# Optimization experiments

Measured on AMD Instinct MI355X. Metric: run time of the kernel, lower is better.

The kernel has to match this reference:

```python
import jax, jax.numpy as jnp
import numpy as np

N_SPATIAL = 65160
N_SPHERE = 2883
N_EDGES = 131072
D = 256             # latent_size
EDGE_IN_FIRST = 3 + 2 * D   # raw 3-dim displacements + sender + receiver = 515
EDGE_IN_REST = 3 * D        # after step 1 edges are D-dim = 768
NODE_IN = 2 * D
N_STEPS = 3


def _layernorm(x, g, b, eps=1e-5):
    m = jnp.mean(x, axis=-1, keepdims=True)
    v = jnp.var(x, axis=-1, keepdims=True)
    return (x - m) * jax.lax.rsqrt(v + eps) * g + b


def _mlp(x, W1, b1, g, o, W2, b2):
    # Linear -> relu -> LayerNorm -> Linear (matches hk.Sequential)
    h = jax.nn.relu(x @ W1 + b1)
    return _layernorm(h, g, o) @ W2 + b2


def setup_inputs() -> dict:
    key = jax.random.key(0)
    ks = jax.random.split(key, 12)

    def glorot(k, shape):
        return jax.random.normal(k, shape, jnp.float32) / np.sqrt(shape[0]).astype(np.float32)

    nodes = jax.random.normal(ks[0], (N_SPATIAL + N_SPHERE, D), jnp.float32)
    edges = jax.random.normal(ks[1], (N_EDGES, 3), jnp.float32)
    senders = jax.random.randint(ks[2], (N_EDGES,), 0, N_SPATIAL)
    # receivers index into the sphere portion of the concatenated node array
    receivers = jax.random.randint(ks[3], (N_EDGES,), 0, N_SPHERE) + N_SPATIAL
    return {
        "nodes": nodes,
        "edges": edges,
        "senders": senders,
        "receivers": receivers,
        "We1a": glorot(ks[4], (EDGE_IN_FIRST, D)),
        "We1b": glorot(ks[5], (EDGE_IN_REST, D)),
        "be1": jnp.zeros((D,), jnp.float32),
        "ge": jnp.ones((D,), jnp.float32),
        "oe": jnp.zeros((D,), jnp.float32),
        "We2": glorot(ks[6], (D, D)),
        "be2": jnp.zeros((D,), jnp.float32),
        "Wn1": glorot(ks[7], (NODE_IN, D)),
        "bn1": jnp.zeros((D,), jnp.float32),
        "gn": jnp.ones((D,), jnp.float32),
        "on": jnp.zeros((D,), jnp.float32),
        "Wn2": glorot(ks[8], (D, D)),
        "bn2": jnp.zeros((D,), jnp.float32),
        "n_spatial": N_SPATIAL,
        "n_sphere": N_SPHERE,
    }


def reference(nodes, edges, senders, receivers,
              We1a, We1b, be1, ge, oe, We2, be2,
              Wn1, bn1, gn, on, Wn2, bn2,
              n_spatial, n_sphere):
    recv_ids = receivers - n_spatial  # local sphere indices in [0, n_sphere)
    for step in range(N_STEPS):
        s = nodes[senders]                                   # [E, D]
        r = nodes[receivers]                                 # [E, D]
        edge_in = jnp.concatenate([edges, s, r], axis=1)     # [E, 3+2D] or [E, 3D]
        W1 = We1a if step == 0 else We1b
        edges = _mlp(edge_in, W1, be1, ge, oe, We2, be2)     # [E, D]
        messages = jax.ops.segment_sum(edges, recv_ids, num_segments=n_sphere)  # [S, D]
        sphere = nodes[n_spatial:]                           # [S, D]
        node_in = jnp.concatenate([sphere, messages], axis=1)
        updated = _mlp(node_in, Wn1, bn1, gn, on, Wn2, bn2)  # [S, D]
        nodes = jnp.concatenate([nodes[:n_spatial], updated], axis=0)
    return nodes[n_spatial:]
```

## Files before the change

kernel.cpp:

```cpp
#include <hip/hip_runtime.h>
#include <hip/hip_bf16.h>
#include <cstdint>
#include <cstddef>

#define N_SPATIAL_C 65160
#define N_SPHERE_C  2883
#define N_EDGES_C   131072

typedef short bf16x8 __attribute__((ext_vector_type(8)));
typedef float f32x4  __attribute__((ext_vector_type(4)));

__device__ inline float bf2f(ushort u) {
    union { uint u; float f; } c; c.u = ((uint)u) << 16; return c.f;
}
__device__ inline ushort f2bf(float f) {
    __hip_bfloat16 h = __float2bfloat16(f);
    union { __hip_bfloat16 h; ushort u; } c; c.h = h; return c.u;
}

template<int EPI, int KI, typename OutT>
__global__ __launch_bounds__(256, 2) void mfma_gemm(
    const ushort* __restrict__ A, const ushort* __restrict__ Bt,
    OutT* __restrict__ C, int M,
    const float* __restrict__ bias,
    const float* __restrict__ g, const float* __restrict__ o,
    const ushort* __restrict__ P, const int* __restrict__ senders,
    const float* __restrict__ Rf, const int* __restrict__ receivers)
{
    constexpr int CHR = KI / 8;
    __shared__ __align__(16) ushort Atile[64 * KI];

    const int m0   = blockIdx.x * 64;
    const int t    = threadIdx.x;
    const int w    = t >> 6;
    const int lane = t & 63;
    const int lo   = lane & 15, hi = lane >> 4, sw = lo & 7;
    const int bn   = w * 64;

#pragma unroll
    for (int i = 0; i < (64 * CHR) / 256; ++i) {
        int ci = i * 256 + t;
        int r  = ci / CHR;
        int cs = ci % CHR;
        int cg = cs ^ (r & 7);
        int rg = m0 + r; if (rg >= M) rg = M - 1;
        const ushort* gp = A + (size_t)rg * KI + cg * 8;
        const ushort* lp = Atile + (size_t)(i * 256 + w * 64) * 8;
        __builtin_amdgcn_global_load_lds(
            (const __attribute__((address_space(1))) unsigned int*)gp,
            (__attribute__((address_space(3))) unsigned int*)lp, 16, 0, 0);
    }
    __syncthreads();

    f32x4 acc[4][4];
#pragma unroll
    for (int rt = 0; rt < 4; ++rt)
#pragma unroll
        for (int ct = 0; ct < 4; ++ct)
#pragma unroll
            for (int j = 0; j < 4; ++j) acc[rt][ct][j] = 0.f;

#pragma unroll
    for (int ks = 0; ks < KI / 32; ++ks) {
        bf16x8 av[4], bv[4];
#pragma unroll
        for (int rt = 0; rt < 4; ++rt) {
            int row = rt * 16 + lo;
            av[rt] = *reinterpret_cast<const bf16x8*>(
                Atile + ((size_t)row * CHR + ((ks * 4 + hi) ^ sw)) * 8);
        }
#pragma unroll
        for (int ct = 0; ct < 4; ++ct)
            bv[ct] = *reinterpret_cast<const bf16x8*>(
                Bt + (size_t)(bn + ct * 16 + lo) * KI + ks * 32 + hi * 8);
#pragma unroll
        for (int rt = 0; rt < 4; ++rt)
#pragma unroll
            for (int ct = 0; ct < 4; ++ct)
                acc[rt][ct] = __builtin_amdgcn_mfma_f32_16x16x32_bf16(
                    av[rt], bv[ct], acc[rt][ct], 0, 0, 0);
    }

    float* xbuf = reinterpret_cast<float*>(Atile);
    const int rl = t >> 4, q = t & 15, c0 = q * 16;

#pragma unroll
    for (int ph = 0; ph < 4; ++ph) {
        __syncthreads();
#pragma unroll
        for (int ct = 0; ct < 4; ++ct)
#pragma unroll
            for (int reg = 0; reg < 4; ++reg)
                xbuf[(size_t)(hi * 4 + reg) * 260 + (bn + ct * 16 + lo)] =
                    acc[ph][ct][reg];
        __syncthreads();

        int rowg = m0 + ph * 16 + rl;
        bool ok  = rowg < M;
        int rowc = ok ? rowg : M - 1;

        float x[16];
#pragma unroll
        for (int jj = 0; jj < 4; ++jj) {
            f32x4 v = *reinterpret_cast<const f32x4*>(xbuf + (size_t)rl * 260 + c0 + jj * 4);
            x[jj*4+0] = v[0]; x[jj*4+1] = v[1]; x[jj*4+2] = v[2]; x[jj*4+3] = v[3];
        }
        if (bias) {
#pragma unroll
            for (int jj = 0; jj < 4; ++jj) {
                f32x4 v = *reinterpret_cast<const f32x4*>(bias + c0 + jj * 4);
                x[jj*4+0] += v[0]; x[jj*4+1] += v[1]; x[jj*4+2] += v[2]; x[jj*4+3] += v[3];
            }
        }
        if (EPI == 2) {
            int sIdx = senders[rowc];
            int rIdx = receivers[rowc] - N_SPATIAL_C;
            bf16x8 p0 = *reinterpret_cast<const bf16x8*>(P + (size_t)sIdx * 256 + c0);
            bf16x8 p1 = *reinterpret_cast<const bf16x8*>(P + (size_t)sIdx * 256 + c0 + 8);
#pragma unroll
            for (int j = 0; j < 8; ++j) {
                x[j]     += bf2f((ushort)p0[j]);
                x[8 + j] += bf2f((ushort)p1[j]);
            }
#pragma unroll
            for (int jj = 0; jj < 4; ++jj) {
                f32x4 v = *reinterpret_cast<const f32x4*>(Rf + (size_t)rIdx * 256 + c0 + jj * 4);
                x[jj*4+0] += v[0]; x[jj*4+1] += v[1]; x[jj*4+2] += v[2]; x[jj*4+3] += v[3];
            }
        }
        if (EPI >= 1) {
#pragma unroll
            for (int j = 0; j < 16; ++j) x[j] = fmaxf(x[j], 0.f);
            float s1 = 0.f, s2 = 0.f;
#pragma unroll
            for (int j = 0; j < 16; ++j) { s1 += x[j]; s2 += x[j] * x[j]; }
#pragma unroll
            for (int m = 1; m < 16; m <<= 1) {
                s1 += __shfl_xor(s1, m);
                s2 += __shfl_xor(s2, m);
            }
            float mean = s1 * (1.f / 256.f);
            float var  = s2 * (1.f / 256.f) - mean * mean;
            float rstd = rsqrtf(var + 1e-5f);
            float gg[16], oo[16];
#pragma unroll
            for (int jj = 0; jj < 4; ++jj) {
                f32x4 gv = *reinterpret_cast<const f32x4*>(g + c0 + jj * 4);
                f32x4 ov = *reinterpret_cast<const f32x4*>(o + c0 + jj * 4);
                gg[jj*4+0]=gv[0]; gg[jj*4+1]=gv[1]; gg[jj*4+2]=gv[2]; gg[jj*4+3]=gv[3];
                oo[jj*4+0]=ov[0]; oo[jj*4+1]=ov[1]; oo[jj*4+2]=ov[2]; oo[jj*4+3]=ov[3];
            }
#pragma unroll
            for (int j = 0; j < 16; ++j)
                x[j] = (x[j] - mean) * rstd * gg[j] + oo[j];
        }
        if (ok) {
            if constexpr (sizeof(OutT) == 2) {
                bf16x8 s0, s1;
#pragma unroll
                for (int j = 0; j < 8; ++j) {
                    s0[j] = (short)f2bf(x[j]);
                    s1[j] = (short)f2bf(x[8 + j]);
                }
                ushort* Cp = (ushort*)C + (size_t)rowg * 256 + c0;
                *reinterpret_cast<bf16x8*>(Cp)     = s0;
                *reinterpret_cast<bf16x8*>(Cp + 8) = s1;
            } else {
                float* Cp = (float*)C + (size_t)rowg * 256 + c0;
#pragma unroll
                for (int jj = 0; jj < 4; ++jj) {
                    f32x4 v;
                    v[0]=x[jj*4+0]; v[1]=x[jj*4+1]; v[2]=x[jj*4+2]; v[3]=x[jj*4+3];
                    *reinterpret_cast<f32x4*>(Cp + jj * 4) = v;
                }
            }
        }
    }
}

__global__ __launch_bounds__(256) void fuse0(
    const float* __restrict__ edges3, const float* __restrict__ Ae,
    const ushort* __restrict__ P, const int* __restrict__ senders,
    const float* __restrict__ Rf, const int* __restrict__ receivers,
    const float* __restrict__ be1, const float* __restrict__ g,
    const float* __restrict__ o, ushort* __restrict__ H)
{
    int row  = blockIdx.x * 4 + (threadIdx.x >> 6);
    int lane = threadIdx.x & 63;
    int c = lane * 4;

    float e0 = edges3[(size_t)row * 3 + 0];
    float e1 = edges3[(size_t)row * 3 + 1];
    float e2 = edges3[(size_t)row * 3 + 2];
    int s = senders[row];
    int r = receivers[row] - N_SPATIAL_C;
    ushort4 pv = *reinterpret_cast<const ushort4*>(P + (size_t)s * 256 + c);
    float4  rv = *reinterpret_cast<const float4*>(Rf + (size_t)r * 256 + c);

    float pw[4] = {bf2f(pv.x), bf2f(pv.y), bf2f(pv.z), bf2f(pv.w)};
    float rw[4] = {rv.x, rv.y, rv.z, rv.w};
    float x[4];
#pragma unroll
    for (int j = 0; j < 4; ++j) {
        x[j] = e0 * Ae[c + j] + e1 * Ae[256 + c + j] + e2 * Ae[512 + c + j]
             + be1[c + j] + pw[j] + rw[j];
        x[j] = fmaxf(x[j], 0.f);
    }
    float s1 = x[0] + x[1] + x[2] + x[3];
    float s2 = x[0]*x[0] + x[1]*x[1] + x[2]*x[2] + x[3]*x[3];
#pragma unroll
    for (int m = 32; m > 0; m >>= 1) { s1 += __shfl_xor(s1, m); s2 += __shfl_xor(s2, m); }
    float mean = s1 * (1.f / 256.f);
    float var  = s2 * (1.f / 256.f) - mean * mean;
    float rstd = rsqrtf(var + 1e-5f);
#pragma unroll
    for (int j = 0; j < 4; ++j) {
        float y = (x[j] - mean) * rstd * g[c + j] + o[c + j];
        H[(size_t)row * 256 + c + j] = f2bf(y);
    }
}

__global__ void count_k(const int* __restrict__ receivers, int* __restrict__ cnt)
{
    int e = blockIdx.x * 256 + threadIdx.x;
    if (e < N_EDGES_C) atomicAdd(&cnt[receivers[e] - N_SPATIAL_C], 1);
}

__global__ void scan_k(const int* __restrict__ cnt, int* __restrict__ row_start)
{
    __shared__ int sums[257];
    const int CH = 12;
    int t = threadIdx.x;
    int local = 0;
    for (int i = 0; i < CH; ++i) {
        int idx = t * CH + i;
        if (idx < N_SPHERE_C) local += cnt[idx];
    }
    sums[t] = local;
    __syncthreads();
    if (t == 0) {
        int run = 0;
        for (int i = 0; i < 256; ++i) { int v = sums[i]; sums[i] = run; run += v; }
        sums[256] = run;
    }
    __syncthreads();
    int base = sums[t];
    for (int i = 0; i < CH; ++i) {
        int idx = t * CH + i;
        if (idx < N_SPHERE_C) { row_start[idx] = base; base += cnt[idx]; }
    }
    if (t == 0) row_start[N_SPHERE_C] = sums[256];
}

__global__ void fill_k(const int* __restrict__ receivers, const int* __restrict__ row_start,
                       int* __restrict__ cursor, int* __restrict__ csr)
{
    int e = blockIdx.x * 256 + threadIdx.x;
    if (e < N_EDGES_C) {
        int rid = receivers[e] - N_SPATIAL_C;
        int pos = atomicAdd(&cursor[rid], 1);
        csr[row_start[rid] + pos] = e;
    }
}

__global__ __launch_bounds__(256) void seg_gather(
    const ushort* __restrict__ H, const int* __restrict__ row_start,
    const int* __restrict__ csr, ushort* __restrict__ S)
{
    __shared__ float red[3][64][4];
    int n = blockIdx.x;
    int sub = threadIdx.x >> 6, l = threadIdx.x & 63, c = l * 4;
    int beg = row_start[n], end = row_start[n + 1];
    float a0 = 0.f, a1 = 0.f, a2 = 0.f, a3 = 0.f;
    for (int i = beg + sub; i < end; i += 4) {
        int e = csr[i];
        ushort4 v = *reinterpret_cast<const ushort4*>(H + (size_t)e * 256 + c);
        a0 += bf2f(v.x); a1 += bf2f(v.y); a2 += bf2f(v.z); a3 += bf2f(v.w);
    }
    if (sub) { red[sub-1][l][0]=a0; red[sub-1][l][1]=a1; red[sub-1][l][2]=a2; red[sub-1][l][3]=a3; }
    __syncthreads();
    if (sub == 0) {
#pragma unroll
        for (int s_ = 0; s_ < 3; ++s_) {
            a0 += red[s_][l][0]; a1 += red[s_][l][1];
            a2 += red[s_][l][2]; a3 += red[s_][l][3];
        }
        ushort4 u; u.x = f2bf(a0); u.y = f2bf(a1); u.z = f2bf(a2); u.w = f2bf(a3);
        *reinterpret_cast<ushort4*>(S + (size_t)n * 256 + c) = u;
    }
}

__global__ void node_assemble(const ushort* __restrict__ sphere, const float* __restrict__ Mmsg,
                              const int* __restrict__ cnt, const float* __restrict__ be2,
                              ushort* __restrict__ node_in)
{
    int n = blockIdx.x, d = threadIdx.x;
    node_in[(size_t)n * 512 + d] = sphere[(size_t)n * 256 + d];
    node_in[(size_t)n * 512 + 256 + d] =
        f2bf(Mmsg[(size_t)n * 256 + d] + (float)cnt[n] * be2[d]);
}

__global__ __launch_bounds__(256) void wf_kernel(
    const float* __restrict__ We2, const float* __restrict__ Be, ushort* __restrict__ Wft)
{
    __shared__ float colB[256];
    int j = blockIdx.x, k = threadIdx.x;
    colB[k] = Be[(size_t)k * 256 + j];
    __syncthreads();
    const float* wrow = We2 + (size_t)k * 256;
    float acc = 0.f;
    for (int t = 0; t < 256; ++t) acc += wrow[t] * colB[t];
    Wft[(size_t)j * 256 + k] = f2bf(acc);
}

__global__ void bf_kernel(const float* __restrict__ be1, const float* __restrict__ be2,
                          const float* __restrict__ Be, float* __restrict__ bfc)
{
    int j = threadIdx.x;
    float acc = be1[j];
    for (int k = 0; k < 256; ++k) acc += be2[k] * Be[(size_t)k * 256 + j];
    bfc[j] = acc;
}

__global__ void tcast(const float* __restrict__ W, ushort* __restrict__ Wt, int K)
{
    __shared__ float tbuf[16][17];
    int k0 = blockIdx.x * 16, n0 = blockIdx.y * 16;
    int tx = threadIdx.x, ty = threadIdx.y;
    tbuf[ty][tx] = W[(size_t)(k0 + ty) * 256 + n0 + tx];
    __syncthreads();
    Wt[(size_t)(n0 + ty) * K + k0 + tx] = f2bf(tbuf[tx][ty]);
}

__global__ void cast_f32_bf16(const float* __restrict__ src, ushort* __restrict__ dst, int n4)
{
    int i = blockIdx.x * 256 + threadIdx.x;
    if (i < n4) {
        float4 v = *reinterpret_cast<const float4*>(src + (size_t)i * 4);
        ushort4 u;
        u.x = f2bf(v.x); u.y = f2bf(v.y); u.z = f2bf(v.z); u.w = f2bf(v.w);
        *reinterpret_cast<ushort4*>(dst + (size_t)i * 4) = u;
    }
}

extern "C" void kernel_launch(void* const* d_in, const int* in_sizes, int n_in,
                              void* d_out, int out_size, void* d_ws, size_t ws_size,
                              hipStream_t stream)
{
    const float* nodes     = (const float*)d_in[0];
    const float* edges3    = (const float*)d_in[1];
    const int*   senders   = (const int*)d_in[2];
    const int*   receivers = (const int*)d_in[3];
    const float* We1a      = (const float*)d_in[4];
    const float* We1b      = (const float*)d_in[5];
    const float* be1       = (const float*)d_in[6];
    const float* ge        = (const float*)d_in[7];
    const float* oe        = (const float*)d_in[8];
    const float* We2       = (const float*)d_in[9];
    const float* be2       = (const float*)d_in[10];
    const float* Wn1       = (const float*)d_in[11];
    const float* bn1       = (const float*)d_in[12];
    const float* gn        = (const float*)d_in[13];
    const float* on_       = (const float*)d_in[14];
    const float* Wn2       = (const float*)d_in[15];
    const float* bn2       = (const float*)d_in[16];

    const float* Ae  = We1a;
    const float* As_ = We1a + 3 * 256;
    const float* Ar  = We1a + 259 * 256;
    const float* Be  = We1b;
    const float* Bs_ = We1b + 256 * 256;
    const float* Br  = We1b + 512 * 256;

    char* ws = (char*)d_ws;
    size_t off = 0;
    auto alloc = [&](size_t b) -> char* {
        char* p = ws + off;
        off += (b + 255) & ~(size_t)255;
        return p;
    };
    ushort* H          = (ushort*)alloc((size_t)N_EDGES_C * 256 * 2);
    ushort* Pb         = (ushort*)alloc((size_t)N_SPATIAL_C * 256 * 2);
    ushort* nodes_bf   = (ushort*)alloc((size_t)N_SPATIAL_C * 256 * 2);
    float*  Rf         = (float*)alloc((size_t)N_SPHERE_C * 256 * 4);
    ushort* sphere_bf  = (ushort*)alloc((size_t)N_SPHERE_C * 256 * 2);
    ushort* S_bf       = (ushort*)alloc((size_t)N_SPHERE_C * 256 * 2);
    ushort* nH         = (ushort*)alloc((size_t)N_SPHERE_C * 256 * 2);
    ushort* node_in_bf = (ushort*)alloc((size_t)N_SPHERE_C * 512 * 2);
    float*  Mmsg       = (float*)alloc((size_t)N_SPHERE_C * 256 * 4);
    ushort* Ast  = (ushort*)alloc(256 * 256 * 2);
    ushort* Art  = (ushort*)alloc(256 * 256 * 2);
    ushort* Bst  = (ushort*)alloc(256 * 256 * 2);
    ushort* Brt  = (ushort*)alloc(256 * 256 * 2);
    ushort* We2t = (ushort*)alloc(256 * 256 * 2);
    ushort* Wn2t = (ushort*)alloc(256 * 256 * 2);
    ushort* Wn1t = (ushort*)alloc(512 * 256 * 2);
    ushort* Wft  = (ushort*)alloc(256 * 256 * 2);
    float*  bfc  = (float*)alloc(256 * 4);
    int* cnt       = (int*)alloc(N_SPHERE_C * 4);
    int* cursor    = (int*)alloc(N_SPHERE_C * 4);
    int* row_start = (int*)alloc((N_SPHERE_C + 1) * 4);
    int* csr       = (int*)alloc((size_t)N_EDGES_C * 4);

    hipMemsetAsync(cnt, 0, N_SPHERE_C * 4, stream);
    hipMemsetAsync(cursor, 0, N_SPHERE_C * 4, stream);
    count_k<<<(N_EDGES_C + 255) / 256, 256, 0, stream>>>(receivers, cnt);
    scan_k<<<1, 256, 0, stream>>>(cnt, row_start);
    fill_k<<<(N_EDGES_C + 255) / 256, 256, 0, stream>>>(receivers, row_start, cursor, csr);

    dim3 tb(16, 16);
    tcast<<<dim3(16, 16), tb, 0, stream>>>(As_, Ast, 256);
    tcast<<<dim3(16, 16), tb, 0, stream>>>(Ar,  Art, 256);
    tcast<<<dim3(16, 16), tb, 0, stream>>>(Bs_, Bst, 256);
    tcast<<<dim3(16, 16), tb, 0, stream>>>(Br,  Brt, 256);
    tcast<<<dim3(16, 16), tb, 0, stream>>>(We2, We2t, 256);
    tcast<<<dim3(16, 16), tb, 0, stream>>>(Wn2, Wn2t, 256);
    tcast<<<dim3(32, 16), tb, 0, stream>>>(Wn1, Wn1t, 512);
    wf_kernel<<<256, 256, 0, stream>>>(We2, Be, Wft);
    bf_kernel<<<1, 256, 0, stream>>>(be1, be2, Be, bfc);

    cast_f32_bf16<<<(N_SPATIAL_C * 64 + 255) / 256, 256, 0, stream>>>(
        nodes, nodes_bf, N_SPATIAL_C * 64);
    cast_f32_bf16<<<(N_SPHERE_C * 64 + 255) / 256, 256, 0, stream>>>(
        nodes + (size_t)N_SPATIAL_C * 256, sphere_bf, N_SPHERE_C * 64);

    const int GE = N_EDGES_C / 64;
    const int GP = (N_SPATIAL_C + 63) / 64;
    const int GS = (N_SPHERE_C + 63) / 64;

    mfma_gemm<0, 256, ushort><<<GP, 256, 0, stream>>>(
        nodes_bf, Ast, Pb, N_SPATIAL_C,
        nullptr, nullptr, nullptr, nullptr, nullptr, nullptr, nullptr);

    for (int step = 0; step < 3; ++step) {
        mfma_gemm<0, 256, float><<<GS, 256, 0, stream>>>(
            sphere_bf, step == 0 ? Art : Brt, Rf, N_SPHERE_C,
            nullptr, nullptr, nullptr, nullptr, nullptr, nullptr, nullptr);

        if (step == 0) {
            fuse0<<<N_EDGES_C / 4, 256, 0, stream>>>(
                edges3, Ae, Pb, senders, Rf, receivers, be1, ge, oe, H);
            mfma_gemm<0, 256, ushort><<<GP, 256, 0, stream>>>(
                nodes_bf, Bst, Pb, N_SPATIAL_C,
                nullptr, nullptr, nullptr, nullptr, nullptr, nullptr, nullptr);
        } else {
            mfma_gemm<2, 256, ushort><<<GE, 256, 0, stream>>>(
                H, Wft, H, N_EDGES_C,
                bfc, ge, oe, Pb, senders, Rf, receivers);
        }

        seg_gather<<<N_SPHERE_C, 256, 0, stream>>>(H, row_start, csr, S_bf);
        mfma_gemm<0, 256, float><<<GS, 256, 0, stream>>>(
            S_bf, We2t, Mmsg, N_SPHERE_C,
            nullptr, nullptr, nullptr, nullptr, nullptr, nullptr, nullptr);
        node_assemble<<<N_SPHERE_C, 256, 0, stream>>>(sphere_bf, Mmsg, cnt, be2, node_in_bf);

        mfma_gemm<1, 512, ushort><<<GS, 256, 0, stream>>>(
            node_in_bf, Wn1t, nH, N_SPHERE_C,
            bn1, gn, on_, nullptr, nullptr, nullptr, nullptr);
        if (step < 2) {
            mfma_gemm<0, 256, ushort><<<GS, 256, 0, stream>>>(
                nH, Wn2t, sphere_bf, N_SPHERE_C,
                bn2, nullptr, nullptr, nullptr, nullptr, nullptr, nullptr);
        } else {
            mfma_gemm<0, 256, float><<<GS, 256, 0, stream>>>(
                nH, Wn2t, (float*)d_out, N_SPHERE_C,
                bn2, nullptr, nullptr, nullptr, nullptr, nullptr, nullptr);
        }
    }
}
```

Measured before the change: 677.6 us.

## Make big GEMMs persistent with double-buffered A tiles and fold message GEMM into node MLP

The large GEMMs (spatial projections and the edge MLP) now run as persistent kernels over a fixed 512-block grid. Each block keeps its B fragments in registers and double-buffers A tiles in LDS, with explicit waitcnt and barriers so the next tile's load overlaps the current tile's compute. Separately, the We2 message projection is folded algebraically into the node-MLP first-layer weights, with a count-weighted bias vector added in the epilogue. seg_gather and the weight GEMMs now write straight into a strided node_in buffer, which removes the Mmsg GEMM, node_assemble, and extra copies. The costs are higher register and LDS pressure and possible bf16 rounding changes from the precomputed weight product.

```diff
diff --git a/kernel.cpp b/kernel.cpp
--- a/kernel.cpp
+++ b/kernel.cpp
@@ -18,163 +18,217 @@
     union { __hip_bfloat16 h; ushort u; } c; c.h = h; return c.u;
 }
 
-template<int EPI, int KI, typename OutT>
+#define VMWAIT8()  asm volatile("s_waitcnt vmcnt(8)" ::: "memory")
+#define VMWAIT0()  asm volatile("s_waitcnt vmcnt(0)" ::: "memory")
+#define LGKM0()    asm volatile("s_waitcnt lgkmcnt(0)" ::: "memory")
+#define SBAR()     do { __builtin_amdgcn_sched_barrier(0); \
+                        __builtin_amdgcn_s_barrier(); \
+                        __builtin_amdgcn_sched_barrier(0); } while (0)
+
+template<int EPI, int KI, int NBUF, typename OutT>
 __global__ __launch_bounds__(256, 2) void mfma_gemm(
     const ushort* __restrict__ A, const ushort* __restrict__ Bt,
-    OutT* __restrict__ C, int M,
+    OutT* __restrict__ C, int M, int lda, int ldc,
     const float* __restrict__ bias,
     const float* __restrict__ g, const float* __restrict__ o,
     const ushort* __restrict__ P, const int* __restrict__ senders,
-    const float* __restrict__ Rf, const int* __restrict__ receivers)
+    const float* __restrict__ Rf, const int* __restrict__ receivers,
+    const int* __restrict__ cntv, const float* __restrict__ bxv)
 {
     constexpr int CHR = KI / 8;
-    __shared__ __align__(16) ushort Atile[64 * KI];
-
-    const int m0   = blockIdx.x * 64;
+    __shared__ __align__(16) ushort lds[NBUF][64 * KI];
+
+    const int nt = (M + 63) >> 6;
+    if ((int)blockIdx.x >= nt) return;
+    const int G    = gridDim.x;
     const int t    = threadIdx.x;
     const int w    = t >> 6;
     const int lane = t & 63;
     const int lo   = lane & 15, hi = lane >> 4, sw = lo & 7;
     const int bn   = w * 64;
-
-#pragma unroll
-    for (int i = 0; i < (64 * CHR) / 256; ++i) {
-        int ci = i * 256 + t;
-        int r  = ci / CHR;
-        int cs = ci % CHR;
-        int cg = cs ^ (r & 7);
-        int rg = m0 + r; if (rg >= M) rg = M - 1;
-        const ushort* gp = A + (size_t)rg * KI + cg * 8;
-        const ushort* lp = Atile + (size_t)(i * 256 + w * 64) * 8;
-        __builtin_amdgcn_global_load_lds(
-            (const __attribute__((address_space(1))) unsigned int*)gp,
-            (__attribute__((address_space(3))) unsigned int*)lp, 16, 0, 0);
-    }
-    __syncthreads();
-
-    f32x4 acc[4][4];
-#pragma unroll
-    for (int rt = 0; rt < 4; ++rt)
-#pragma unroll
-        for (int ct = 0; ct < 4; ++ct)
-#pragma unroll
-            for (int j = 0; j < 4; ++j) acc[rt][ct][j] = 0.f;
-
-#pragma unroll
-    for (int ks = 0; ks < KI / 32; ++ks) {
-        bf16x8 av[4], bv[4];
-#pragma unroll
-        for (int rt = 0; rt < 4; ++rt) {
-            int row = rt * 16 + lo;
-            av[rt] = *reinterpret_cast<const bf16x8*>(
-                Atile + ((size_t)row * CHR + ((ks * 4 + hi) ^ sw)) * 8);
-        }
-#pragma unroll
-        for (int ct = 0; ct < 4; ++ct)
-            bv[ct] = *reinterpret_cast<const bf16x8*>(
-                Bt + (size_t)(bn + ct * 16 + lo) * KI + ks * 32 + hi * 8);
+    const int rl   = t >> 4, q = t & 15, c0 = q * 16;
+
+    auto STAGE = [&](int buf, int tileIdx) {
+#pragma unroll
+        for (int i = 0; i < (64 * CHR) / 256; ++i) {
+            int ci = i * 256 + t;
+            int r  = ci / CHR;
+            int cs = ci % CHR;
+            int cg = cs ^ (r & 7);
+            int rg = tileIdx * 64 + r; if (rg >= M) rg = M - 1;
+            const ushort* gp = A + (size_t)rg * lda + cg * 8;
+            const ushort* lp = &lds[buf][(size_t)(i * 256 + w * 64) * 8];
+            __builtin_amdgcn_global_load_lds(
+                (const __attribute__((address_space(1))) unsigned int*)gp,
+                (__attribute__((address_space(3))) unsigned int*)lp, 16, 0, 0);
+        }
+    };
+
+    bf16x8 breg[(NBUF == 2) ? 8 : 1][4];
+    if constexpr (NBUF == 2) {
+#pragma unroll
+        for (int ks = 0; ks < 8; ++ks)
+#pragma unroll
+            for (int ct = 0; ct < 4; ++ct)
+                breg[ks][ct] = *reinterpret_cast<const bf16x8*>(
+                    Bt + (size_t)(bn + ct * 16 + lo) * KI + ks * 32 + hi * 8);
+        STAGE(0, blockIdx.x);
+    }
+
+    int cur = 0;
+    for (int tt = blockIdx.x; tt < nt; tt += G) {
+        if constexpr (NBUF == 1) {
+            STAGE(0, tt);
+            VMWAIT0();
+        } else {
+            int tn = tt + G;
+            if (tn < nt) { STAGE(cur ^ 1, tn); VMWAIT8(); }
+            else         { VMWAIT0(); }
+        }
+        SBAR();
+
+        const ushort* At = lds[cur];
+        f32x4 acc[4][4];
 #pragma unroll
         for (int rt = 0; rt < 4; ++rt)
 #pragma unroll
             for (int ct = 0; ct < 4; ++ct)
-                acc[rt][ct] = __builtin_amdgcn_mfma_f32_16x16x32_bf16(
-                    av[rt], bv[ct], acc[rt][ct], 0, 0, 0);
-    }
-
-    float* xbuf = reinterpret_cast<float*>(Atile);
-    const int rl = t >> 4, q = t & 15, c0 = q * 16;
-
-#pragma unroll
-    for (int ph = 0; ph < 4; ++ph) {
-        __syncthreads();
-#pragma unroll
-        for (int ct = 0; ct < 4; ++ct)
-#pragma unroll
-            for (int reg = 0; reg < 4; ++reg)
-                xbuf[(size_t)(hi * 4 + reg) * 260 + (bn + ct * 16 + lo)] =
-                    acc[ph][ct][reg];
-        __syncthreads();
-
-        int rowg = m0 + ph * 16 + rl;
-        bool ok  = rowg < M;
-        int rowc = ok ? rowg : M - 1;
-
-        float x[16];
-#pragma unroll
-        for (int jj = 0; jj < 4; ++jj) {
-            f32x4 v = *reinterpret_cast<const f32x4*>(xbuf + (size_t)rl * 260 + c0 + jj * 4);
-            x[jj*4+0] = v[0]; x[jj*4+1] = v[1]; x[jj*4+2] = v[2]; x[jj*4+3] = v[3];
-        }
-        if (bias) {
+#pragma unroll
+                for (int j = 0; j < 4; ++j) acc[rt][ct][j] = 0.f;
+
+#pragma unroll
+        for (int ks = 0; ks < KI / 32; ++ks) {
+            bf16x8 av[4], bv[4];
+#pragma unroll
+            for (int rt = 0; rt < 4; ++rt) {
+                int row = rt * 16 + lo;
+                av[rt] = *reinterpret_cast<const bf16x8*>(
+                    At + ((size_t)row * CHR + ((ks * 4 + hi) ^ sw)) * 8);
+            }
+            if constexpr (NBUF == 2) {
+#pragma unroll
+                for (int ct = 0; ct < 4; ++ct) bv[ct] = breg[ks][ct];
+            } else {
+#pragma unroll
+                for (int ct = 0; ct < 4; ++ct)
+                    bv[ct] = *reinterpret_cast<const bf16x8*>(
+                        Bt + (size_t)(bn + ct * 16 + lo) * KI + ks * 32 + hi * 8);
+            }
+#pragma unroll
+            for (int rt = 0; rt < 4; ++rt)
+#pragma unroll
+                for (int ct = 0; ct < 4; ++ct)
+                    acc[rt][ct] = __builtin_amdgcn_mfma_f32_16x16x32_bf16(
+                        av[rt], bv[ct], acc[rt][ct], 0, 0, 0);
+        }
+
+        float* xbuf = (float*)lds[cur];
+#pragma unroll
+        for (int ph = 0; ph < 4; ++ph) {
+            LGKM0(); SBAR();
+#pragma unroll
+            for (int ct = 0; ct < 4; ++ct)
+#pragma unroll
+                for (int reg = 0; reg < 4; ++reg)
+                    xbuf[(size_t)(hi * 4 + reg) * 260 + (bn + ct * 16 + lo)] =
+                        acc[ph][ct][reg];
+            LGKM0(); SBAR();
+
+            int rowg = tt * 64 + ph * 16 + rl;
+            bool ok  = rowg < M;
+            int rowc = ok ? rowg : M - 1;
+
+            float x[16];
 #pragma unroll
             for (int jj = 0; jj < 4; ++jj) {
-                f32x4 v = *reinterpret_cast<const f32x4*>(bias + c0 + jj * 4);
-                x[jj*4+0] += v[0]; x[jj*4+1] += v[1]; x[jj*4+2] += v[2]; x[jj*4+3] += v[3];
-            }
-        }
-        if (EPI == 2) {
-            int sIdx = senders[rowc];
-            int rIdx = receivers[rowc] - N_SPATIAL_C;
-            bf16x8 p0 = *reinterpret_cast<const bf16x8*>(P + (size_t)sIdx * 256 + c0);
-            bf16x8 p1 = *reinterpret_cast<const bf16x8*>(P + (size_t)sIdx * 256 + c0 + 8);
-#pragma unroll
-            for (int j = 0; j < 8; ++j) {
-                x[j]     += bf2f((ushort)p0[j]);
-                x[8 + j] += bf2f((ushort)p1[j]);
-            }
-#pragma unroll
-            for (int jj = 0; jj < 4; ++jj) {
-                f32x4 v = *reinterpret_cast<const f32x4*>(Rf + (size_t)rIdx * 256 + c0 + jj * 4);
-                x[jj*4+0] += v[0]; x[jj*4+1] += v[1]; x[jj*4+2] += v[2]; x[jj*4+3] += v[3];
-            }
-        }
-        if (EPI >= 1) {
-#pragma unroll
-            for (int j = 0; j < 16; ++j) x[j] = fmaxf(x[j], 0.f);
-            float s1 = 0.f, s2 = 0.f;
-#pragma unroll
-            for (int j = 0; j < 16; ++j) { s1 += x[j]; s2 += x[j] * x[j]; }
-#pragma unroll
-            for (int m = 1; m < 16; m <<= 1) {
-                s1 += __shfl_xor(s1, m);
-                s2 += __shfl_xor(s2, m);
-            }
-            float mean = s1 * (1.f / 256.f);
-            float var  = s2 * (1.f / 256.f) - mean * mean;
-            float rstd = rsqrtf(var + 1e-5f);
-            float gg[16], oo[16];
-#pragma unroll
-            for (int jj = 0; jj < 4; ++jj) {
-                f32x4 gv = *reinterpret_cast<const f32x4*>(g + c0 + jj * 4);
-                f32x4 ov = *reinterpret_cast<const f32x4*>(o + c0 + jj * 4);
-                gg[jj*4+0]=gv[0]; gg[jj*4+1]=gv[1]; gg[jj*4+2]=gv[2]; gg[jj*4+3]=gv[3];
-                oo[jj*4+0]=ov[0]; oo[jj*4+1]=ov[1]; oo[jj*4+2]=ov[2]; oo[jj*4+3]=ov[3];
-            }
-#pragma unroll
-            for (int j = 0; j < 16; ++j)
-                x[j] = (x[j] - mean) * rstd * gg[j] + oo[j];
-        }
-        if (ok) {
-            if constexpr (sizeof(OutT) == 2) {
-                bf16x8 s0, s1;
+                f32x4 v = *reinterpret_cast<const f32x4*>(
+                    xbuf + (size_t)rl * 260 + c0 + jj * 4);
+                x[jj*4+0] = v[0]; x[jj*4+1] = v[1];
+                x[jj*4+2] = v[2]; x[jj*4+3] = v[3];
+            }
+            if (bias) {
+#pragma unroll
+                for (int jj = 0; jj < 4; ++jj) {
+                    f32x4 v = *reinterpret_cast<const f32x4*>(bias + c0 + jj * 4);
+                    x[jj*4+0] += v[0]; x[jj*4+1] += v[1];
+                    x[jj*4+2] += v[2]; x[jj*4+3] += v[3];
+                }
+            }
+            if (EPI == 1 && cntv) {
+                float cf = (float)cntv[rowc];
+#pragma unroll
+                for (int jj = 0; jj < 4; ++jj) {
+                    f32x4 v = *reinterpret_cast<const f32x4*>(bxv + c0 + jj * 4);
+                    x[jj*4+0] += cf * v[0]; x[jj*4+1] += cf * v[1];
+                    x[jj*4+2] += cf * v[2]; x[jj*4+3] += cf * v[3];
+                }
+            }
+            if (EPI == 2) {
+                int sIdx = senders[rowc];
+                int rIdx = receivers[rowc] - N_SPATIAL_C;
+                bf16x8 p0 = *reinterpret_cast<const bf16x8*>(P + (size_t)sIdx * 256 + c0);
+                bf16x8 p1 = *reinterpret_cast<const bf16x8*>(P + (size_t)sIdx * 256 + c0 + 8);
 #pragma unroll
                 for (int j = 0; j < 8; ++j) {
-                    s0[j] = (short)f2bf(x[j]);
-                    s1[j] = (short)f2bf(x[8 + j]);
-                }
-                ushort* Cp = (ushort*)C + (size_t)rowg * 256 + c0;
-                *reinterpret_cast<bf16x8*>(Cp)     = s0;
-                *reinterpret_cast<bf16x8*>(Cp + 8) = s1;
-            } else {
-                float* Cp = (float*)C + (size_t)rowg * 256 + c0;
+                    x[j]     += bf2f((ushort)p0[j]);
+                    x[8 + j] += bf2f((ushort)p1[j]);
+                }
 #pragma unroll
                 for (int jj = 0; jj < 4; ++jj) {
-                    f32x4 v;
-                    v[0]=x[jj*4+0]; v[1]=x[jj*4+1]; v[2]=x[jj*4+2]; v[3]=x[jj*4+3];
-                    *reinterpret_cast<f32x4*>(Cp + jj * 4) = v;
-                }
-            }
-        }
+                    f32x4 v = *reinterpret_cast<const f32x4*>(
+                        Rf + (size_t)rIdx * 256 + c0 + jj * 4);
+                    x[jj*4+0] += v[0]; x[jj*4+1] += v[1];
+                    x[jj*4+2] += v[2]; x[jj*4+3] += v[3];
+                }
+            }
+            if (EPI >= 1) {
+#pragma unroll
+                for (int j = 0; j < 16; ++j) x[j] = fmaxf(x[j], 0.f);
+                float s1 = 0.f, s2 = 0.f;
+#pragma unroll
+                for (int j = 0; j < 16; ++j) { s1 += x[j]; s2 += x[j] * x[j]; }
+#pragma unroll
+                for (int m = 1; m < 16; m <<= 1) {
+                    s1 += __shfl_xor(s1, m);
+                    s2 += __shfl_xor(s2, m);
+                }
+                float mean = s1 * (1.f / 256.f);
+                float var  = s2 * (1.f / 256.f) - mean * mean;
+                float rstd = rsqrtf(var + 1e-5f);
+#pragma unroll
+                for (int jj = 0; jj < 4; ++jj) {
+                    f32x4 gv = *reinterpret_cast<const f32x4*>(g + c0 + jj * 4);
+                    f32x4 ov = *reinterpret_cast<const f32x4*>(o + c0 + jj * 4);
+#pragma unroll
+                    for (int e = 0; e < 4; ++e)
+                        x[jj*4+e] = (x[jj*4+e] - mean) * rstd * gv[e] + ov[e];
+                }
+            }
+            if (ok) {
+                if constexpr (sizeof(OutT) == 2) {
+                    bf16x8 s0, s1v;
+#pragma unroll
+                    for (int j = 0; j < 8; ++j) {
+                        s0[j]  = (short)f2bf(x[j]);
+                        s1v[j] = (short)f2bf(x[8 + j]);
+                    }
+                    ushort* Cp = (ushort*)C + (size_t)rowg * ldc + c0;
+                    *reinterpret_cast<bf16x8*>(Cp)     = s0;
+                    *reinterpret_cast<bf16x8*>(Cp + 8) = s1v;
+                } else {
+                    float* Cp = (float*)C + (size_t)rowg * ldc + c0;
+#pragma unroll
+                    for (int jj = 0; jj < 4; ++jj) {
+                        f32x4 v;
+                        v[0]=x[jj*4+0]; v[1]=x[jj*4+1];
+                        v[2]=x[jj*4+2]; v[3]=x[jj*4+3];
+                        *reinterpret_cast<f32x4*>(Cp + jj * 4) = v;
+                    }
+                }
+            }
+        }
+        LGKM0(); SBAR();
+        if constexpr (NBUF == 2) cur ^= 1;
     }
 }
 
@@ -265,7 +319,7 @@
 
 __global__ __launch_bounds__(256) void seg_gather(
     const ushort* __restrict__ H, const int* __restrict__ row_start,
-    const int* __restrict__ csr, ushort* __restrict__ S)
+    const int* __restrict__ csr, ushort* __restrict__ S, int ldS)
 {
     __shared__ float red[3][64][4];
     int n = blockIdx.x;
@@ -286,50 +340,41 @@
             a2 += red[s_][l][2]; a3 += red[s_][l][3];
         }
         ushort4 u; u.x = f2bf(a0); u.y = f2bf(a1); u.z = f2bf(a2); u.w = f2bf(a3);
-        *reinterpret_cast<ushort4*>(S + (size_t)n * 256 + c) = u;
-    }
-}
-
-__global__ void node_assemble(const ushort* __restrict__ sphere, const float* __restrict__ Mmsg,
-                              const int* __restrict__ cnt, const float* __restrict__ be2,
-                              ushort* __restrict__ node_in)
-{
-    int n = blockIdx.x, d = threadIdx.x;
-    node_in[(size_t)n * 512 + d] = sphere[(size_t)n * 256 + d];
-    node_in[(size_t)n * 512 + 256 + d] =
-        f2bf(Mmsg[(size_t)n * 256 + d] + (float)cnt[n] * be2[d]);
-}
-
-__global__ __launch_bounds__(256) void wf_kernel(
-    const float* __restrict__ We2, const float* __restrict__ Be, ushort* __restrict__ Wft)
+        *reinterpret_cast<ushort4*>(S + (size_t)n * ldS + c) = u;
+    }
+}
+
+__global__ __launch_bounds__(256) void wprod_kernel(
+    const float* __restrict__ We2, const float* __restrict__ Bsrc,
+    ushort* __restrict__ Wt, int ldd, int koff)
 {
     __shared__ float colB[256];
     int j = blockIdx.x, k = threadIdx.x;
-    colB[k] = Be[(size_t)k * 256 + j];
+    colB[k] = Bsrc[(size_t)k * 256 + j];
     __syncthreads();
     const float* wrow = We2 + (size_t)k * 256;
     float acc = 0.f;
     for (int t = 0; t < 256; ++t) acc += wrow[t] * colB[t];
-    Wft[(size_t)j * 256 + k] = f2bf(acc);
-}
-
-__global__ void bf_kernel(const float* __restrict__ be1, const float* __restrict__ be2,
-                          const float* __restrict__ Be, float* __restrict__ bfc)
+    Wt[(size_t)j * ldd + koff + k] = f2bf(acc);
+}
+
+__global__ void bvecprod_kernel(const float* __restrict__ base, const float* __restrict__ bvec,
+                                const float* __restrict__ W, float* __restrict__ bout)
 {
     int j = threadIdx.x;
-    float acc = be1[j];
-    for (int k = 0; k < 256; ++k) acc += be2[k] * Be[(size_t)k * 256 + j];
-    bfc[j] = acc;
-}
-
-__global__ void tcast(const float* __restrict__ W, ushort* __restrict__ Wt, int K)
+    float acc = base ? base[j] : 0.f;
+    for (int k = 0; k < 256; ++k) acc += bvec[k] * W[(size_t)k * 256 + j];
+    bout[j] = acc;
+}
+
+__global__ void tcast2(const float* __restrict__ W, ushort* __restrict__ Wt, int ldd)
 {
     __shared__ float tbuf[16][17];
     int k0 = blockIdx.x * 16, n0 = blockIdx.y * 16;
     int tx = threadIdx.x, ty = threadIdx.y;
     tbuf[ty][tx] = W[(size_t)(k0 + ty) * 256 + n0 + tx];
     __syncthreads();
-    Wt[(size_t)(n0 + ty) * K + k0 + tx] = f2bf(tbuf[tx][ty]);
+    Wt[(size_t)(n0 + ty) * ldd + k0 + tx] = f2bf(tbuf[tx][ty]);
 }
 
 __global__ void cast_f32_bf16(const float* __restrict__ src, ushort* __restrict__ dst, int n4)
@@ -341,6 +386,13 @@
         u.x = f2bf(v.x); u.y = f2bf(v.y); u.z = f2bf(v.z); u.w = f2bf(v.w);
         *reinterpret_cast<ushort4*>(dst + (size_t)i * 4) = u;
     }
+}
+
+__global__ void cast_sphere(const float* __restrict__ nodes, ushort* __restrict__ node_in)
+{
+    int n = blockIdx.x, d = threadIdx.x;
+    node_in[(size_t)n * 512 + d] =
+        f2bf(nodes[(size_t)(N_SPATIAL_C + n) * 256 + d]);
 }
 
 extern "C" void kernel_launch(void* const* d_in, const int* in_sizes, int n_in,
@@ -371,6 +423,7 @@
     const float* Be  = We1b;
     const float* Bs_ = We1b + 256 * 256;
     const float* Br  = We1b + 512 * 256;
+    const float* Wn1bot = Wn1 + 256 * 256;
 
     char* ws = (char*)d_ws;
     size_t off = 0;
@@ -383,20 +436,17 @@
     ushort* Pb         = (ushort*)alloc((size_t)N_SPATIAL_C * 256 * 2);
     ushort* nodes_bf   = (ushort*)alloc((size_t)N_SPATIAL_C * 256 * 2);
     float*  Rf         = (float*)alloc((size_t)N_SPHERE_C * 256 * 4);
-    ushort* sphere_bf  = (ushort*)alloc((size_t)N_SPHERE_C * 256 * 2);
-    ushort* S_bf       = (ushort*)alloc((size_t)N_SPHERE_C * 256 * 2);
+    ushort* node_in_bf = (ushort*)alloc((size_t)N_SPHERE_C * 512 * 2);
     ushort* nH         = (ushort*)alloc((size_t)N_SPHERE_C * 256 * 2);
-    ushort* node_in_bf = (ushort*)alloc((size_t)N_SPHERE_C * 512 * 2);
-    float*  Mmsg       = (float*)alloc((size_t)N_SPHERE_C * 256 * 4);
     ushort* Ast  = (ushort*)alloc(256 * 256 * 2);
     ushort* Art  = (ushort*)alloc(256 * 256 * 2);
     ushort* Bst  = (ushort*)alloc(256 * 256 * 2);
     ushort* Brt  = (ushort*)alloc(256 * 256 * 2);
-    ushort* We2t = (ushort*)alloc(256 * 256 * 2);
     ushort* Wn2t = (ushort*)alloc(256 * 256 * 2);
-    ushort* Wn1t = (ushort*)alloc(512 * 256 * 2);
     ushort* Wft  = (ushort*)alloc(256 * 256 * 2);
+    ushort* Bnt  = (ushort*)alloc(256 * 512 * 2);
     float*  bfc  = (float*)alloc(256 * 4);
+    float*  bxv  = (float*)alloc(256 * 4);
     int* cnt       = (int*)alloc(N_SPHERE_C * 4);
     int* cursor    = (int*)alloc(N_SPHERE_C * 4);
     int* row_start = (int*)alloc((N_SPHERE_C + 1) * 4);
@@ -409,63 +459,62 @@
     fill_k<<<(N_EDGES_C + 255) / 256, 256, 0, stream>>>(receivers, row_start, cursor, csr);
 
     dim3 tb(16, 16);
-    tcast<<<dim3(16, 16), tb, 0, stream>>>(As_, Ast, 256);
-    tcast<<<dim3(16, 16), tb, 0, stream>>>(Ar,  Art, 256);
-    tcast<<<dim3(16, 16), tb, 0, stream>>>(Bs_, Bst, 256);
-    tcast<<<dim3(16, 16), tb, 0, stream>>>(Br,  Brt, 256);
-    tcast<<<dim3(16, 16), tb, 0, stream>>>(We2, We2t, 256);
-    tcast<<<dim3(16, 16), tb, 0, stream>>>(Wn2, Wn2t, 256);
-    tcast<<<dim3(32, 16), tb, 0, stream>>>(Wn1, Wn1t, 512);
-    wf_kernel<<<256, 256, 0, stream>>>(We2, Be, Wft);
-    bf_kernel<<<1, 256, 0, stream>>>(be1, be2, Be, bfc);
+    tcast2<<<dim3(16, 16), tb, 0, stream>>>(As_, Ast, 256);
+    tcast2<<<dim3(16, 16), tb, 0, stream>>>(Ar,  Art, 256);
+    tcast2<<<dim3(16, 16), tb, 0, stream>>>(Bs_, Bst, 256);
+    tcast2<<<dim3(16, 16), tb, 0, stream>>>(Br,  Brt, 256);
+    tcast2<<<dim3(16, 16), tb, 0, stream>>>(Wn2, Wn2t, 256);
+    tcast2<<<dim3(16, 16), tb, 0, stream>>>(Wn1, Bnt, 512);
+    wprod_kernel<<<256, 256, 0, stream>>>(We2, Be, Wft, 256, 0);
+    wprod_kernel<<<256, 256, 0, stream>>>(We2, Wn1bot, Bnt, 512, 256);
+    bvecprod_kernel<<<1, 256, 0, stream>>>(be1, be2, Be, bfc);
+    bvecprod_kernel<<<1, 256, 0, stream>>>(nullptr, be2, Wn1bot, bxv);
 
     cast_f32_bf16<<<(N_SPATIAL_C * 64 + 255) / 256, 256, 0, stream>>>(
         nodes, nodes_bf, N_SPATIAL_C * 64);
-    cast_f32_bf16<<<(N_SPHERE_C * 64 + 255) / 256, 256, 0, stream>>>(
-        nodes + (size_t)N_SPATIAL_C * 256, sphere_bf, N_SPHERE_C * 64);
-
-    const int GE = N_EDGES_C / 64;
-    const int GP = (N_SPATIAL_C + 63) / 64;
+    cast_sphere<<<N_SPHERE_C, 256, 0, stream>>>(nodes, node_in_bf);
+
+    const int GBIG = 512;
     const int GS = (N_SPHERE_C + 63) / 64;
 
-    mfma_gemm<0, 256, ushort><<<GP, 256, 0, stream>>>(
-        nodes_bf, Ast, Pb, N_SPATIAL_C,
-        nullptr, nullptr, nullptr, nullptr, nullptr, nullptr, nullptr);
+    const float* nul = nullptr;
+
+    mfma_gemm<0, 256, 2, ushort><<<GBIG, 256, 0, stream>>>(
+        nodes_bf, Ast, Pb, N_SPATIAL_C, 256, 256,
+        nul, nul, nul, nullptr, nullptr, nul, nullptr, nullptr, nul);
 
     for (int step = 0; step < 3; ++step) {
-        mfma_gemm<0, 256, float><<<GS, 256, 0, stream>>>(
-            sphere_bf, step == 0 ? Art : Brt, Rf, N_SPHERE_C,
-            nullptr, nullptr, nullptr, nullptr, nullptr, nullptr, nullptr);
+        mfma_gemm<0, 256, 2, float><<<GS, 256, 0, stream>>>(
+            node_in_bf, step == 0 ? Art : Brt, Rf, N_SPHERE_C, 512, 256,
+            nul, nul, nul, nullptr, nullptr, nul, nullptr, nullptr, nul);
 
         if (step == 0) {
             fuse0<<<N_EDGES_C / 4, 256, 0, stream>>>(
                 edges3, Ae, Pb, senders, Rf, receivers, be1, ge, oe, H);
-            mfma_gemm<0, 256, ushort><<<GP, 256, 0, stream>>>(
-                nodes_bf, Bst, Pb, N_SPATIAL_C,
-                nullptr, nullptr, nullptr, nullptr, nullptr, nullptr, nullptr);
+            mfma_gemm<0, 256, 2, ushort><<<GBIG, 256, 0, stream>>>(
+                nodes_bf, Bst, Pb, N_SPATIAL_C, 256, 256,
+                nul, nul, nul, nullptr, nullptr, nul, nullptr, nullptr, nul);
         } else {
-            mfma_gemm<2, 256, ushort><<<GE, 256, 0, stream>>>(
-                H, Wft, H, N_EDGES_C,
-                bfc, ge, oe, Pb, senders, Rf, receivers);
-        }
-
-        seg_gather<<<N_SPHERE_C, 256, 0, stream>>>(H, row_start, csr, S_bf);
-        mfma_gemm<0, 256, float><<<GS, 256, 0, stream>>>(
-            S_bf, We2t, Mmsg, N_SPHERE_C,
-            nullptr, nullptr, nullptr, nullptr, nullptr, nullptr, nullptr);
-        node_assemble<<<N_SPHERE_C, 256, 0, stream>>>(sphere_bf, Mmsg, cnt, be2, node_in_bf);
-
-        mfma_gemm<1, 512, ushort><<<GS, 256, 0, stream>>>(
-            node_in_bf, Wn1t, nH, N_SPHERE_C,
-            bn1, gn, on_, nullptr, nullptr, nullptr, nullptr);
+            mfma_gemm<2, 256, 2, ushort><<<GBIG, 256, 0, stream>>>(
+                H, Wft, H, N_EDGES_C, 256, 256,
+                bfc, ge, oe, Pb, senders, Rf, receivers, nullptr, nul);
+        }
+
+        seg_gather<<<N_SPHERE_C, 256, 0, stream>>>(H, row_start, csr,
+                                                   node_in_bf + 256, 512);
+
+        mfma_gemm<1, 512, 1, ushort><<<GS, 256, 0, stream>>>(
+            node_in_bf, Bnt, nH, N_SPHERE_C, 512, 256,
+            bn1, gn, on_, nullptr, nullptr, nul, nullptr, cnt, bxv);
+
         if (step < 2) {
-            mfma_gemm<0, 256, ushort><<<GS, 256, 0, stream>>>(
-                nH, Wn2t, sphere_bf, N_SPHERE_C,
-                bn2, nullptr, nullptr, nullptr, nullptr, nullptr, nullptr);
+            mfma_gemm<0, 256, 2, ushort><<<GS, 256, 0, stream>>>(
+                nH, Wn2t, node_in_bf, N_SPHERE_C, 256, 512,
+                bn2, nul, nul, nullptr, nullptr, nul, nullptr, nullptr, nul);
         } else {
-            mfma_gemm<0, 256, float><<<GS, 256, 0, stream>>>(
-                nH, Wn2t, (float*)d_out, N_SPHERE_C,
-                bn2, nullptr, nullptr, nullptr, nullptr, nullptr, nullptr);
-        }
-    }
-}
+            mfma_gemm<0, 256, 2, float><<<GS, 256, 0, stream>>>(
+                nH, Wn2t, (float*)d_out, N_SPHERE_C, 256, 256,
+                bn2, nul, nul, nullptr, nullptr, nul, nullptr, nullptr, nul);
+        }
+    }
+}
```

Result: no change. 665.9 us (-1.7%).
